# Optimization experiments

Hardware: AMD Instinct MI355X
Metric: run time of the kernel (lower is better)

Reference implementation:

```python
import jax, jax.numpy as jnp
import numpy as np

LOWRES = 256  # low-res input to coefficient tower
GB = 16       # spatial_bins (grid H=W)
LB = 8        # luma_bins (grid depth)
NIN, NOUT = 3, 3


def _conv_s2(x, w, b):
    # 3x3 stride-2 conv, torch padding=1
    y = jax.lax.conv_general_dilated(x, w, (2, 2), ((1, 1), (1, 1)),
                                     dimension_numbers=('NCHW', 'OIHW', 'NCHW'))
    return y + b[None, :, None, None]


def _pw(x, w, b):
    # 1x1 conv as einsum; w: [O, C]
    return jnp.einsum('bchw,oc->bohw', x, w) + b[None, :, None, None]


def _bilateral_slice(grid, guide, image):
    # grid [B,12,L,GH,GW]; guide [B,H,W] in [0,1]; image [B,NIN,H,W]
    B, C, L, GH, GW = grid.shape
    H, W = guide.shape[1], guide.shape[2]
    cx = (jnp.arange(W, dtype=jnp.float32) + 0.5) * (GW / W) - 0.5
    cy = (jnp.arange(H, dtype=jnp.float32) + 0.5) * (GH / H) - 0.5
    cz = guide * L - 0.5
    x0f = jnp.floor(cx); wx = cx - x0f
    y0f = jnp.floor(cy); wy = cy - y0f
    z0f = jnp.floor(cz); wz = cz - z0f
    x0 = x0f.astype(jnp.int32); y0 = y0f.astype(jnp.int32); z0 = z0f.astype(jnp.int32)
    bidx = jnp.arange(B)[:, None, None]
    acc = jnp.zeros((B, H, W, C), jnp.float32)
    for dz in (0, 1):
        zi = jnp.clip(z0 + dz, 0, L - 1)                     # [B,H,W]
        wzz = wz if dz else (1.0 - wz)
        for dy in (0, 1):
            yi = jnp.clip(y0 + dy, 0, GH - 1)[None, :, None]
            wyy = (wy if dy else (1.0 - wy))[None, :, None]
            for dx in (0, 1):
                xi = jnp.clip(x0 + dx, 0, GW - 1)[None, None, :]
                wxx = (wx if dx else (1.0 - wx))[None, None, :]
                g = grid[bidx, :, zi, yi, xi]                # [B,H,W,C]
                acc = acc + (wzz * wyy * wxx)[..., None] * g
    aff = acc.reshape(B, H, W, NOUT, NIN + 1)
    out = jnp.einsum('bhwci,bihw->bchw', aff[..., :NIN], image) \
        + jnp.transpose(aff[..., NIN], (0, 3, 1, 2))
    return out


def reference(image, val, sw0, sb0, sw1, sb1, sw2, sb2, sw3, sb3, spw, spb,
              lw1, lb1, lw2, lb2, lw3, lb3, cw, cb, fw1, fb1, fw2, fb2,
              gw, gb, ccm_w, ccm_b, shifts, slopes, prw, prb):
    B = image.shape[0]
    low = jax.image.resize(image, (B, NIN, LOWRES, LOWRES), 'bilinear', antialias=False)
    # splat tower: 4 stride-2 3x3 convs + final 1x1 (no relu)
    x = jax.nn.relu(_conv_s2(low, sw0, sb0))
    x = jax.nn.relu(_conv_s2(x, sw1, sb1))
    x = jax.nn.relu(_conv_s2(x, sw2, sb2))
    x = jax.nn.relu(_conv_s2(x, sw3, sb3))           # [B,64,16,16]
    splat = _pw(x, spw, spb) + val                   # + conditioning value
    # local path: three 1x1 convs with relu
    loc = jax.nn.relu(_pw(splat, lw1, lb1))
    loc = jax.nn.relu(_pw(loc, lw2, lb2))
    loc = jax.nn.relu(_pw(loc, lw3, lb3))            # [B,64,16,16]
    # condition path: 1x1 stride-2 conv -> adaptive avgpool(4) -> 2 fc layers
    c = jax.nn.relu(_pw(splat[:, :, ::2, ::2], cw, cb))  # [B,4,8,8]
    c = c.reshape(B, 4, 4, 2, 4, 2).mean(axis=(3, 5))    # [B,4,4,4]
    c = c.reshape(B, 64)
    c = jax.nn.relu(c @ fw1.T + fb1)
    c = jax.nn.relu(c @ fw2.T + fb2)                 # [B,64]
    fused = jax.nn.relu(c[:, :, None, None] + loc)
    coeff = _pw(fused, gw, gb)                       # [B,96,16,16]
    # split into LB chunks of 12 along channels, stack at dim 2
    grid = coeff.reshape(B, LB, NOUT * (NIN + 1), GB, GB).transpose(0, 2, 1, 3, 4)
    # guidemap: ccm -> piecewise-linear curve -> projection -> hardtanh [0,1]
    g = _pw(image, ccm_w, ccm_b)                     # [B,3,H,W]
    g = (slopes * jax.nn.relu(g[..., None] - shifts[None])).sum(-1)
    g = _pw(g, prw, prb)[:, 0]                       # [B,H,W]
    guide = jnp.clip(g, 0.0, 1.0)
    return _bilateral_slice(grid, guide, image)


def setup_inputs() -> dict:
    rng = np.random.default_rng(0)
    def rn(shape, fan_in):
        return jnp.asarray(rng.standard_normal(shape).astype(np.float32) * np.sqrt(2.0 / fan_in))
    B, H, W = 4, 1024, 1024
    d = {}
    d['image'] = jnp.asarray(rng.random((B, 3, H, W), dtype=np.float32))
    d['val'] = jnp.asarray(rng.random((B, 1, 1, 1), dtype=np.float32))
    # splat tower 3->8->16->32->64
    chans = [(3, 8), (8, 16), (16, 32), (32, 64)]
    for i, (ci, co) in enumerate(chans):
        d[f'sw{i}'] = rn((co, ci, 3, 3), ci * 9)
        d[f'sb{i}'] = jnp.zeros((co,), jnp.float32)
    d['spw'] = rn((64, 64), 64); d['spb'] = jnp.zeros((64,), jnp.float32)
    d['lw1'] = rn((128, 64), 64); d['lb1'] = jnp.zeros((128,), jnp.float32)
    d['lw2'] = rn((128, 128), 128); d['lb2'] = jnp.zeros((128,), jnp.float32)
    d['lw3'] = rn((64, 128), 128); d['lb3'] = jnp.zeros((64,), jnp.float32)
    d['cw'] = rn((4, 64), 64); d['cb'] = jnp.zeros((4,), jnp.float32)
    d['fw1'] = rn((64, 64), 64); d['fb1'] = jnp.zeros((64,), jnp.float32)
    d['fw2'] = rn((64, 64), 64); d['fb2'] = jnp.zeros((64,), jnp.float32)
    d['gw'] = rn((96, 64), 64); d['gb'] = jnp.zeros((96,), jnp.float32)
    # guide params (mirrors make_guide_params init)
    d['ccm_w'] = jnp.asarray(np.identity(3, dtype=np.float32)
                             + rng.standard_normal((3, 3)).astype(np.float32) * 1e-4)
    d['ccm_b'] = jnp.zeros((3,), jnp.float32)
    shifts = np.linspace(0, 1, 16, endpoint=False, dtype=np.float32)[None, None, None, :]
    d['shifts'] = jnp.asarray(np.tile(shifts, (3, 1, 1, 1)))
    slopes = np.zeros((1, 3, 1, 1, 16), dtype=np.float32); slopes[..., 0] = 1.0
    d['slopes'] = jnp.asarray(slopes)
    d['prw'] = jnp.ones((1, 3), jnp.float32) / 3.0
    d['prb'] = jnp.zeros((1,), jnp.float32)
    return d
```

## Files before the change

### kernel.cpp

```cpp
#include <hip/hip_runtime.h>

#define BATCH 4
#define HH 1024
#define WW 1024

__global__ __launch_bounds__(256) void dsconv0_k(const float* __restrict__ img,
                                                 const float* __restrict__ wgt,
                                                 const float* __restrict__ bias,
                                                 float* __restrict__ out) {
  int blk = blockIdx.x;
  int tx = blk & 7;
  int ty = (blk >> 3) & 7;
  int b = blk >> 6;
  int t = threadIdx.x;

  __shared__ float low[3][33][36];

  int Y0 = ty << 4, X0 = tx << 4;
  int gy0 = 2 * Y0 - 1, gx0 = 2 * X0 - 1;

  for (int i = t; i < 3 * 33 * 33; i += 256) {
    int c = i / 1089;
    int rem = i - c * 1089;
    int ly = rem / 33;
    int lx = rem - ly * 33;
    int gy = gy0 + ly, gx = gx0 + lx;
    float v = 0.f;
    if (gy >= 0 && gx >= 0) {
      const float* p = img + (size_t)(b * 3 + c) * HH * WW + (4 * gy + 1) * WW + 4 * gx + 1;
      v = 0.25f * (p[0] + p[1] + p[WW] + p[WW + 1]);
    }
    low[c][ly][lx] = v;
  }
  __syncthreads();

  int x = t & 15, y = t >> 4;
  float acc[8];
#pragma unroll
  for (int o = 0; o < 8; ++o) acc[o] = bias[o];
  for (int ci = 0; ci < 3; ++ci) {
#pragma unroll
    for (int ky = 0; ky < 3; ++ky) {
#pragma unroll
      for (int kx = 0; kx < 3; ++kx) {
        float v = low[ci][2 * y + ky][2 * x + kx];
#pragma unroll
        for (int o = 0; o < 8; ++o)
          acc[o] += wgt[o * 27 + ci * 9 + ky * 3 + kx] * v;
      }
    }
  }
  float* ob = out + (size_t)b * 8 * 128 * 128 + (Y0 + y) * 128 + X0 + x;
#pragma unroll
  for (int o = 0; o < 8; ++o) ob[o * 128 * 128] = fmaxf(acc[o], 0.f);
}

template <int CI, int CO, int HI, int P>
__global__ __launch_bounds__(256) void conv_tile_k(const float* __restrict__ in,
                                                   const float* __restrict__ wgt,
                                                   const float* __restrict__ bias,
                                                   float* __restrict__ out) {
  const int HO = HI / 2;
  const int NT = HO / P;
  const int HALO = 2 * P + 1;
  const int RS = 2 * P + 4;
  constexpr int NO = (CO * P * P) / 256;
  int blk = blockIdx.x;
  int tx = blk % NT;
  int ty = (blk / NT) % NT;
  int b = blk / (NT * NT);
  int t = threadIdx.x;

  __shared__ float s[CI][HALO][RS];

  int Y0 = ty * P, X0 = tx * P;
  int gy0 = 2 * Y0 - 1, gx0 = 2 * X0 - 1;

  for (int i = t; i < CI * HALO * HALO; i += 256) {
    int c = i / (HALO * HALO);
    int rem = i - c * (HALO * HALO);
    int ly = rem / HALO;
    int lx = rem - ly * HALO;
    int gy = gy0 + ly, gx = gx0 + lx;
    float v = 0.f;
    if (gy >= 0 && gy < HI && gx >= 0 && gx < HI)
      v = in[((size_t)(b * CI + c) * HI + gy) * HI + gx];
    s[c][ly][lx] = v;
  }
  __syncthreads();

  int px = t % (P * P);
  int og = t / (P * P);
  int x = px % P, y = px / P;
  float acc[NO];
#pragma unroll
  for (int j = 0; j < NO; ++j) acc[j] = bias[og * NO + j];
  for (int ci = 0; ci < CI; ++ci) {
#pragma unroll
    for (int ky = 0; ky < 3; ++ky) {
#pragma unroll
      for (int kx = 0; kx < 3; ++kx) {
        float v = s[ci][2 * y + ky][2 * x + kx];
#pragma unroll
        for (int j = 0; j < NO; ++j)
          acc[j] += wgt[((og * NO + j) * CI + ci) * 9 + ky * 3 + kx] * v;
      }
    }
  }
#pragma unroll
  for (int j = 0; j < NO; ++j)
    out[(size_t)(b * CO + og * NO + j) * HO * HO + (Y0 + y) * HO + X0 + x] =
        fmaxf(acc[j], 0.f);
}

__global__ __launch_bounds__(256) void cpfc_k(const float* __restrict__ x3,
                                              const float* __restrict__ spw,
                                              const float* __restrict__ spb,
                                              const float* __restrict__ val,
                                              const float* __restrict__ cw,
                                              const float* __restrict__ cb,
                                              const float* __restrict__ fw1,
                                              const float* __restrict__ fb1,
                                              const float* __restrict__ fw2,
                                              const float* __restrict__ fb2,
                                              float* __restrict__ fc2o) {
  __shared__ float eff[4][64];
  __shared__ float eb[4][4];
  __shared__ float sc[256];
  __shared__ float h1[256];
  int t = threadIdx.x;

  {
    int ch = t >> 6, k = t & 63;
    float a = 0.f;
#pragma unroll 8
    for (int c = 0; c < 64; ++c) a += cw[ch * 64 + c] * spw[c * 64 + k];
    eff[ch][k] = a;
  }
  if (t < 16) {
    int b = t >> 2, ch = t & 3;
    float a = cb[ch];
    float vb = val[b];
#pragma unroll 8
    for (int c = 0; c < 64; ++c) a += cw[ch * 64 + c] * (spb[c] + vb);
    eb[b][ch] = a;
  }
  __syncthreads();

  int b = t >> 6;
  int r = t & 63;
  int ch = r >> 4;
  int py = (r >> 2) & 3;
  int px = r & 3;
  float sum = 0.f;
  for (int dy = 0; dy < 2; ++dy)
    for (int dx = 0; dx < 2; ++dx) {
      int p = (py * 2 + dy) * 32 + (px * 2 + dx) * 2;
      float acc = eb[b][ch];
      const float* xb = x3 + ((size_t)b * 64) * 256 + p;
#pragma unroll 8
      for (int k = 0; k < 64; ++k) acc += eff[ch][k] * xb[k * 256];
      sum += fmaxf(acc, 0.f);
    }
  sc[t] = sum * 0.25f;
  __syncthreads();
  int o = t & 63;
  float acc = fb1[o];
#pragma unroll 8
  for (int k = 0; k < 64; ++k) acc += fw1[o * 64 + k] * sc[b * 64 + k];
  h1[t] = fmaxf(acc, 0.f);
  __syncthreads();
  acc = fb2[o];
#pragma unroll 8
  for (int k = 0; k < 64; ++k) acc += fw2[o * 64 + k] * h1[b * 64 + k];
  fc2o[t] = fmaxf(acc, 0.f);
}

template <int CI, int CO, int RELU>
__device__ __forceinline__ void pw_tile(const float (*__restrict__ X)[36],
                                        float (*__restrict__ Y)[36],
                                        const float* __restrict__ w,
                                        const float* __restrict__ bias,
                                        float badd, int t) {
  constexpr int NO = CO / 32;
  int pg = (t & 7) << 2;
  int og = t >> 3;
  float acc[NO][4];
#pragma unroll
  for (int j = 0; j < NO; ++j) {
    float bb = bias[og * NO + j] + badd;
#pragma unroll
    for (int u = 0; u < 4; ++u) acc[j][u] = bb;
  }
#pragma unroll 4
  for (int k = 0; k < CI; k += 4) {
    float4 xv0 = *(const float4*)&X[k][pg];
    float4 xv1 = *(const float4*)&X[k + 1][pg];
    float4 xv2 = *(const float4*)&X[k + 2][pg];
    float4 xv3 = *(const float4*)&X[k + 3][pg];
#pragma unroll
    for (int j = 0; j < NO; ++j) {
      float4 wv = *(const float4*)&w[(og * NO + j) * CI + k];
      acc[j][0] += wv.x * xv0.x + wv.y * xv1.x + wv.z * xv2.x + wv.w * xv3.x;
      acc[j][1] += wv.x * xv0.y + wv.y * xv1.y + wv.z * xv2.y + wv.w * xv3.y;
      acc[j][2] += wv.x * xv0.z + wv.y * xv1.z + wv.z * xv2.z + wv.w * xv3.z;
      acc[j][3] += wv.x * xv0.w + wv.y * xv1.w + wv.z * xv2.w + wv.w * xv3.w;
    }
  }
#pragma unroll
  for (int j = 0; j < NO; ++j) {
    int o = og * NO + j;
#pragma unroll
    for (int u = 0; u < 4; ++u) {
      float v = acc[j][u];
      if (RELU) v = fmaxf(v, 0.f);
      Y[o][pg + u] = v;
    }
  }
}

__global__ __launch_bounds__(256) void mlp_k(
    const float* __restrict__ x3, const float* __restrict__ spw,
    const float* __restrict__ spb, const float* __restrict__ val,
    const float* __restrict__ lw1, const float* __restrict__ lb1,
    const float* __restrict__ lw2, const float* __restrict__ lb2,
    const float* __restrict__ lw3, const float* __restrict__ lb3,
    const float* __restrict__ fc2o, const float* __restrict__ gw,
    const float* __restrict__ gb, float* __restrict__ gridt) {
  int blk = blockIdx.x;
  int b = blk >> 3;
  int p0 = (blk & 7) << 5;
  int t = threadIdx.x;

  __shared__ float A[128][36];
  __shared__ float Bf[128][36];

  for (int i = t; i < 64 * 32; i += 256) {
    int c = i >> 5, p = i & 31;
    A[c][p] = x3[((size_t)(b * 64 + c)) * 256 + p0 + p];
  }
  __syncthreads();

  pw_tile<64, 64, 0>(A, Bf, spw, spb, val[b], t);
  __syncthreads();
  pw_tile<64, 128, 1>(Bf, A, lw1, lb1, 0.f, t);
  __syncthreads();
  pw_tile<128, 128, 1>(A, Bf, lw2, lb2, 0.f, t);
  __syncthreads();
  pw_tile<128, 64, 1>(Bf, A, lw3, lb3, 0.f, t);
  __syncthreads();

  {
    int pg = (t & 7) << 2;
    int og = t >> 3;
    float acc[3][4];
#pragma unroll
    for (int j = 0; j < 3; ++j) {
      float bb = gb[og * 3 + j];
#pragma unroll
      for (int u = 0; u < 4; ++u) acc[j][u] = bb;
    }
    const float* cv = fc2o + b * 64;
#pragma unroll 4
    for (int k = 0; k < 64; k += 4) {
      float4 cc4 = *(const float4*)&cv[k];
      float4 xv0 = *(const float4*)&A[k][pg];
      float4 xv1 = *(const float4*)&A[k + 1][pg];
      float4 xv2 = *(const float4*)&A[k + 2][pg];
      float4 xv3 = *(const float4*)&A[k + 3][pg];
      xv0.x = fmaxf(xv0.x + cc4.x, 0.f); xv0.y = fmaxf(xv0.y + cc4.x, 0.f);
      xv0.z = fmaxf(xv0.z + cc4.x, 0.f); xv0.w = fmaxf(xv0.w + cc4.x, 0.f);
      xv1.x = fmaxf(xv1.x + cc4.y, 0.f); xv1.y = fmaxf(xv1.y + cc4.y, 0.f);
      xv1.z = fmaxf(xv1.z + cc4.y, 0.f); xv1.w = fmaxf(xv1.w + cc4.y, 0.f);
      xv2.x = fmaxf(xv2.x + cc4.z, 0.f); xv2.y = fmaxf(xv2.y + cc4.z, 0.f);
      xv2.z = fmaxf(xv2.z + cc4.z, 0.f); xv2.w = fmaxf(xv2.w + cc4.z, 0.f);
      xv3.x = fmaxf(xv3.x + cc4.w, 0.f); xv3.y = fmaxf(xv3.y + cc4.w, 0.f);
      xv3.z = fmaxf(xv3.z + cc4.w, 0.f); xv3.w = fmaxf(xv3.w + cc4.w, 0.f);
#pragma unroll
      for (int j = 0; j < 3; ++j) {
        float4 wv = *(const float4*)&gw[(og * 3 + j) * 64 + k];
        acc[j][0] += wv.x * xv0.x + wv.y * xv1.x + wv.z * xv2.x + wv.w * xv3.x;
        acc[j][1] += wv.x * xv0.y + wv.y * xv1.y + wv.z * xv2.y + wv.w * xv3.y;
        acc[j][2] += wv.x * xv0.z + wv.y * xv1.z + wv.z * xv2.z + wv.w * xv3.z;
        acc[j][3] += wv.x * xv0.w + wv.y * xv1.w + wv.z * xv2.w + wv.w * xv3.w;
      }
    }
#pragma unroll
    for (int j = 0; j < 3; ++j) {
      int o = og * 3 + j;
      int l = o / 12, cc = o - l * 12;
#pragma unroll
      for (int u = 0; u < 4; ++u)
        gridt[(size_t)(((b * 8 + l) << 8) + p0 + pg + u) * 12 + cc] = acc[j][u];
    }
  }
}

#define ZST 200
__global__ __launch_bounds__(256) void slice_k(
    const float* __restrict__ img, const float* __restrict__ gridt,
    const float* __restrict__ ccm_w, const float* __restrict__ ccm_b,
    const float* __restrict__ shifts, const float* __restrict__ slopes,
    const float* __restrict__ prw, const float* __restrict__ prb,
    float* __restrict__ out) {
  int blk = blockIdx.x;
  int b = blk >> 10;
  int h = blk & 1023;
  int t = threadIdx.x;

  __shared__ float sg[8 * ZST];
  __shared__ float2 lut[3][16];

  float cy = (h + 0.5f) * 0.015625f - 0.5f;
  float y0f = floorf(cy);
  float wy = cy - y0f;
  int y0 = (int)y0f;
  int yi0 = min(max(y0, 0), 15), yi1 = min(max(y0 + 1, 0), 15);

  if (t < 48) {
    int c = t >> 4, k = t & 15;
    float cs = 0.f, cbv = 0.f;
    for (int i = 0; i <= k; ++i) {
      float s = slopes[c * 16 + i];
      cs += s;
      cbv += s * shifts[c * 16 + i];
    }
    lut[c][k] = make_float2(cs, cbv);
  }

  for (int i = t; i < 384; i += 256) {
    int z = i / 48;
    int e = i - z * 48;
    const float4* s0 =
        (const float4*)(gridt + (size_t)(((b * 8 + z) << 8) + (yi0 << 4)) * 12);
    const float4* s1 =
        (const float4*)(gridt + (size_t)(((b * 8 + z) << 8) + (yi1 << 4)) * 12);
    float4 a = s0[e], c = s1[e];
    float4 v = make_float4(a.x + wy * (c.x - a.x), a.y + wy * (c.y - a.y),
                           a.z + wy * (c.z - a.z), a.w + wy * (c.w - a.w));
    *((float4*)(sg + z * ZST) + e) = v;
  }
  __syncthreads();

  int pp = (h << 10) + (t << 2);
  const float* ib = img + (size_t)b * 3 * HH * WW;
  float4 R4 = *(const float4*)(ib + pp);
  float4 G4 = *(const float4*)(ib + HH * WW + pp);
  float4 B4 = *(const float4*)(ib + 2 * HH * WW + pp);
  float r_[4] = {R4.x, R4.y, R4.z, R4.w};
  float g_[4] = {G4.x, G4.y, G4.z, G4.w};
  float b_[4] = {B4.x, B4.y, B4.z, B4.w};

  float m0 = ccm_w[0], m1 = ccm_w[1], m2 = ccm_w[2];
  float m3 = ccm_w[3], m4 = ccm_w[4], m5 = ccm_w[5];
  float m6 = ccm_w[6], m7 = ccm_w[7], m8 = ccm_w[8];
  float c0 = ccm_b[0], c1 = ccm_b[1], c2 = ccm_b[2];
  float p0 = prw[0], p1 = prw[1], p2 = prw[2], pb = prb[0];

  float base0 = shifts[0], base1 = shifts[16], base2 = shifts[32];
  float inv0 = 1.0f / (shifts[1] - base0);
  float inv1 = 1.0f / (shifts[17] - base1);
  float inv2 = 1.0f / (shifts[33] - base2);

  float ro[4], go[4], bo[4];
#pragma unroll
  for (int j = 0; j < 4; ++j) {
    float r = r_[j], g = g_[j], bl = b_[j];
    float v0 = c0 + m0 * r + m1 * g + m2 * bl;
    float v1 = c1 + m3 * r + m4 * g + m5 * bl;
    float v2 = c2 + m6 * r + m7 * g + m8 * bl;

    float tv0 = fmaxf(v0, base0);
    float tv1 = fmaxf(v1, base1);
    float tv2 = fmaxf(v2, base2);
    int j0 = min((int)((tv0 - base0) * inv0), 15);
    int j1 = min((int)((tv1 - base1) * inv1), 15);
    int j2 = min((int)((tv2 - base2) * inv2), 15);
    float2 e0 = lut[0][j0];
    float2 e1 = lut[1][j1];
    float2 e2 = lut[2][j2];
    float f0 = e0.x * tv0 - e0.y;
    float f1 = e1.x * tv1 - e1.y;
    float f2 = e2.x * tv2 - e2.y;

    float gg = pb + p0 * f0 + p1 * f1 + p2 * f2;
    float guide = fminf(fmaxf(gg, 0.f), 1.f);

    int w = (t << 2) + j;
    float cx = (w + 0.5f) * 0.015625f - 0.5f;
    float x0f = floorf(cx);
    float wx = cx - x0f;
    int x0i = (int)x0f;
    int xi0 = min(max(x0i, 0), 15), xi1 = min(max(x0i + 1, 0), 15);

    float cz = guide * 8.0f - 0.5f;
    float z0f = floorf(cz);
    float wz = cz - z0f;
    int z0i = (int)z0f;
    int zi0 = min(max(z0i, 0), 7), zi1 = min(max(z0i + 1, 0), 7);

    int oz0 = zi0 * ZST, oz1 = zi1 * ZST;
    int ox0 = xi0 * 12, ox1 = xi1 * 12;
    float wz1 = wz, wz0 = 1.f - wz;
    float wx1 = wx, wx0 = 1.f - wx;

    float acc[12];
#pragma unroll
    for (int k = 0; k < 12; ++k) acc[k] = 0.f;

#pragma unroll
    for (int dz = 0; dz < 2; ++dz) {
      int oz = dz ? oz1 : oz0;
      float wzz = dz ? wz1 : wz0;
#pragma unroll
      for (int dx = 0; dx < 2; ++dx) {
        int ox = dx ? ox1 : ox0;
        float wgt = wzz * (dx ? wx1 : wx0);
        const float* gp = sg + oz + ox;
        float4 a0 = *(const float4*)gp;
        float4 a1 = *(const float4*)(gp + 4);
        float4 a2 = *(const float4*)(gp + 8);
        acc[0] += wgt * a0.x;  acc[1] += wgt * a0.y;
        acc[2] += wgt * a0.z;  acc[3] += wgt * a0.w;
        acc[4] += wgt * a1.x;  acc[5] += wgt * a1.y;
        acc[6] += wgt * a1.z;  acc[7] += wgt * a1.w;
        acc[8] += wgt * a2.x;  acc[9] += wgt * a2.y;
        acc[10] += wgt * a2.z; acc[11] += wgt * a2.w;
      }
    }
    ro[j] = acc[0] * r + acc[1] * g + acc[2] * bl + acc[3];
    go[j] = acc[4] * r + acc[5] * g + acc[6] * bl + acc[7];
    bo[j] = acc[8] * r + acc[9] * g + acc[10] * bl + acc[11];
  }
  float* ob = out + (size_t)b * 3 * HH * WW;
  *(float4*)(ob + pp) = make_float4(ro[0], ro[1], ro[2], ro[3]);
  *(float4*)(ob + HH * WW + pp) = make_float4(go[0], go[1], go[2], go[3]);
  *(float4*)(ob + 2 * HH * WW + pp) = make_float4(bo[0], bo[1], bo[2], bo[3]);
}

extern "C" void kernel_launch(void* const* d_in, const int* in_sizes, int n_in,
                              void* d_out, int out_size, void* d_ws, size_t ws_size,
                              hipStream_t stream) {
  const float* image = (const float*)d_in[0];
  const float* val   = (const float*)d_in[1];
  const float* sw0 = (const float*)d_in[2];  const float* sb0 = (const float*)d_in[3];
  const float* sw1 = (const float*)d_in[4];  const float* sb1 = (const float*)d_in[5];
  const float* sw2 = (const float*)d_in[6];  const float* sb2 = (const float*)d_in[7];
  const float* sw3 = (const float*)d_in[8];  const float* sb3 = (const float*)d_in[9];
  const float* spw = (const float*)d_in[10]; const float* spb = (const float*)d_in[11];
  const float* lw1 = (const float*)d_in[12]; const float* lb1 = (const float*)d_in[13];
  const float* lw2 = (const float*)d_in[14]; const float* lb2 = (const float*)d_in[15];
  const float* lw3 = (const float*)d_in[16]; const float* lb3 = (const float*)d_in[17];
  const float* cw  = (const float*)d_in[18]; const float* cb  = (const float*)d_in[19];
  const float* fw1 = (const float*)d_in[20]; const float* fb1 = (const float*)d_in[21];
  const float* fw2 = (const float*)d_in[22]; const float* fb2 = (const float*)d_in[23];
  const float* gw  = (const float*)d_in[24]; const float* gb  = (const float*)d_in[25];
  const float* ccm_w = (const float*)d_in[26]; const float* ccm_b = (const float*)d_in[27];
  const float* shifts = (const float*)d_in[28]; const float* slopes = (const float*)d_in[29];
  const float* prw = (const float*)d_in[30]; const float* prb = (const float*)d_in[31];
  float* out = (float*)d_out;

  float* ws    = (float*)d_ws;
  float* x0    = ws;
  float* x1    = x0 + 524288;
  float* x2    = x1 + 262144;
  float* x3    = x2 + 131072;
  float* fc2o  = x3 + 65536;
  float* gridt = fc2o + 256;

  dsconv0_k<<<256, 256, 0, stream>>>(image, sw0, sb0, x0);
  conv_tile_k<8, 16, 128, 8><<<256, 256, 0, stream>>>(x0, sw1, sb1, x1);
  conv_tile_k<16, 32, 64, 4><<<256, 256, 0, stream>>>(x1, sw2, sb2, x2);
  conv_tile_k<32, 64, 32, 2><<<256, 256, 0, stream>>>(x2, sw3, sb3, x3);
  cpfc_k<<<1, 256, 0, stream>>>(x3, spw, spb, val, cw, cb, fw1, fb1, fw2, fb2,
                                fc2o);
  mlp_k<<<32, 256, 0, stream>>>(x3, spw, spb, val, lw1, lb1, lw2, lb2, lw3, lb3,
                                fc2o, gw, gb, gridt);
  slice_k<<<4096, 256, 0, stream>>>(image, gridt, ccm_w, ccm_b, shifts, slopes,
                                    prw, prb, out);
}
```

Measured before the change: 276.7 us.

## Parallelize global-feature conv/pool across blocks and fuse FC layers into MLP kernel

Replaces the single-block cpfc kernel with a 16-block cpool kernel, one block per (batch, channel), that splits the 64-wide reductions across four thread groups and then sums them. The two small fully-connected layers are moved into mlp_k, where each block recomputes them redundantly and overlaps them with the pointwise tile work. The aim is to shorten a serial, single-block stage on the critical path. The cost is duplicated FC work in all 32 mlp blocks and extra shared-memory reductions and syncs.

```diff
diff --git a/kernel.cpp b/kernel.cpp
--- a/kernel.cpp
+++ b/kernel.cpp
@@ -113,67 +113,62 @@
         fmaxf(acc[j], 0.f);
 }
 
-__global__ __launch_bounds__(256) void cpfc_k(const float* __restrict__ x3,
-                                              const float* __restrict__ spw,
-                                              const float* __restrict__ spb,
-                                              const float* __restrict__ val,
-                                              const float* __restrict__ cw,
-                                              const float* __restrict__ cb,
-                                              const float* __restrict__ fw1,
-                                              const float* __restrict__ fb1,
-                                              const float* __restrict__ fw2,
-                                              const float* __restrict__ fb2,
-                                              float* __restrict__ fc2o) {
-  __shared__ float eff[4][64];
-  __shared__ float eb[4][4];
-  __shared__ float sc[256];
-  __shared__ float h1[256];
+__global__ __launch_bounds__(256) void cpool_k(const float* __restrict__ x3,
+                                               const float* __restrict__ spw,
+                                               const float* __restrict__ spb,
+                                               const float* __restrict__ val,
+                                               const float* __restrict__ cw,
+                                               const float* __restrict__ cb,
+                                               float* __restrict__ cvec) {
+  int blk = blockIdx.x;
+  int ch = blk & 3, b = blk >> 2;
   int t = threadIdx.x;
+  int k = t & 63, q = t >> 6;
+
+  __shared__ float red[4][64];
+  __shared__ float red2[4];
+  __shared__ float effs[64];
+  __shared__ float s8[64];
+  __shared__ float ebs;
 
   {
-    int ch = t >> 6, k = t & 63;
     float a = 0.f;
-#pragma unroll 8
-    for (int c = 0; c < 64; ++c) a += cw[ch * 64 + c] * spw[c * 64 + k];
-    eff[ch][k] = a;
-  }
+#pragma unroll
+    for (int o = q * 16; o < q * 16 + 16; ++o)
+      a += cw[ch * 64 + o] * spw[o * 64 + k];
+    red[q][k] = a;
+  }
+  if (k == 0) {
+    float a = 0.f;
+    float vb = val[b];
+#pragma unroll
+    for (int o = q * 16; o < q * 16 + 16; ++o)
+      a += cw[ch * 64 + o] * (spb[o] + vb);
+    red2[q] = a;
+  }
+  __syncthreads();
+  if (t < 64) effs[t] = red[0][t] + red[1][t] + red[2][t] + red[3][t];
+  if (t == 0) ebs = cb[ch] + red2[0] + red2[1] + red2[2] + red2[3];
+  __syncthreads();
+
+  {
+    int p = ((k >> 3) << 5) + ((k & 7) << 1);
+    float a = 0.f;
+#pragma unroll
+    for (int kk = q * 16; kk < q * 16 + 16; ++kk)
+      a += effs[kk] * x3[((size_t)(b * 64 + kk)) * 256 + p];
+    red[q][k] = a;
+  }
+  __syncthreads();
+  if (t < 64)
+    s8[t] = fmaxf(red[0][t] + red[1][t] + red[2][t] + red[3][t] + ebs, 0.f);
+  __syncthreads();
   if (t < 16) {
-    int b = t >> 2, ch = t & 3;
-    float a = cb[ch];
-    float vb = val[b];
-#pragma unroll 8
-    for (int c = 0; c < 64; ++c) a += cw[ch * 64 + c] * (spb[c] + vb);
-    eb[b][ch] = a;
-  }
-  __syncthreads();
-
-  int b = t >> 6;
-  int r = t & 63;
-  int ch = r >> 4;
-  int py = (r >> 2) & 3;
-  int px = r & 3;
-  float sum = 0.f;
-  for (int dy = 0; dy < 2; ++dy)
-    for (int dx = 0; dx < 2; ++dx) {
-      int p = (py * 2 + dy) * 32 + (px * 2 + dx) * 2;
-      float acc = eb[b][ch];
-      const float* xb = x3 + ((size_t)b * 64) * 256 + p;
-#pragma unroll 8
-      for (int k = 0; k < 64; ++k) acc += eff[ch][k] * xb[k * 256];
-      sum += fmaxf(acc, 0.f);
-    }
-  sc[t] = sum * 0.25f;
-  __syncthreads();
-  int o = t & 63;
-  float acc = fb1[o];
-#pragma unroll 8
-  for (int k = 0; k < 64; ++k) acc += fw1[o * 64 + k] * sc[b * 64 + k];
-  h1[t] = fmaxf(acc, 0.f);
-  __syncthreads();
-  acc = fb2[o];
-#pragma unroll 8
-  for (int k = 0; k < 64; ++k) acc += fw2[o * 64 + k] * h1[b * 64 + k];
-  fc2o[t] = fmaxf(acc, 0.f);
+    int py = t >> 2, px = t & 3;
+    int i0 = (py * 2) * 8 + px * 2;
+    cvec[b * 64 + ch * 16 + t] =
+        0.25f * (s8[i0] + s8[i0 + 1] + s8[i0 + 8] + s8[i0 + 9]);
+  }
 }
 
 template <int CI, int CO, int RELU>
@@ -225,7 +220,9 @@
     const float* __restrict__ lw1, const float* __restrict__ lb1,
     const float* __restrict__ lw2, const float* __restrict__ lb2,
     const float* __restrict__ lw3, const float* __restrict__ lb3,
-    const float* __restrict__ fc2o, const float* __restrict__ gw,
+    const float* __restrict__ cvec, const float* __restrict__ fw1,
+    const float* __restrict__ fb1, const float* __restrict__ fw2,
+    const float* __restrict__ fb2, const float* __restrict__ gw,
     const float* __restrict__ gb, float* __restrict__ gridt) {
   int blk = blockIdx.x;
   int b = blk >> 3;
@@ -234,15 +231,29 @@
 
   __shared__ float A[128][36];
   __shared__ float Bf[128][36];
-
+  __shared__ float scv[64], h1v[64], f2v[64];
+
+  if (t < 64) scv[t] = cvec[b * 64 + t];
   for (int i = t; i < 64 * 32; i += 256) {
     int c = i >> 5, p = i & 31;
     A[c][p] = x3[((size_t)(b * 64 + c)) * 256 + p0 + p];
   }
   __syncthreads();
 
+  if (t < 64) {
+    float a = fb1[t];
+#pragma unroll 8
+    for (int k = 0; k < 64; ++k) a += fw1[t * 64 + k] * scv[k];
+    h1v[t] = fmaxf(a, 0.f);
+  }
   pw_tile<64, 64, 0>(A, Bf, spw, spb, val[b], t);
   __syncthreads();
+  if (t < 64) {
+    float a = fb2[t];
+#pragma unroll 8
+    for (int k = 0; k < 64; ++k) a += fw2[t * 64 + k] * h1v[k];
+    f2v[t] = fmaxf(a, 0.f);
+  }
   pw_tile<64, 128, 1>(Bf, A, lw1, lb1, 0.f, t);
   __syncthreads();
   pw_tile<128, 128, 1>(A, Bf, lw2, lb2, 0.f, t);
@@ -260,10 +271,9 @@
 #pragma unroll
       for (int u = 0; u < 4; ++u) acc[j][u] = bb;
     }
-    const float* cv = fc2o + b * 64;
 #pragma unroll 4
     for (int k = 0; k < 64; k += 4) {
-      float4 cc4 = *(const float4*)&cv[k];
+      float4 cc4 = *(const float4*)&f2v[k];
       float4 xv0 = *(const float4*)&A[k][pg];
       float4 xv1 = *(const float4*)&A[k + 1][pg];
       float4 xv2 = *(const float4*)&A[k + 2][pg];
@@ -465,17 +475,16 @@
   float* x1    = x0 + 524288;
   float* x2    = x1 + 262144;
   float* x3    = x2 + 131072;
-  float* fc2o  = x3 + 65536;
-  float* gridt = fc2o + 256;
+  float* cvec  = x3 + 65536;
+  float* gridt = cvec + 256;
 
   dsconv0_k<<<256, 256, 0, stream>>>(image, sw0, sb0, x0);
   conv_tile_k<8, 16, 128, 8><<<256, 256, 0, stream>>>(x0, sw1, sb1, x1);
   conv_tile_k<16, 32, 64, 4><<<256, 256, 0, stream>>>(x1, sw2, sb2, x2);
   conv_tile_k<32, 64, 32, 2><<<256, 256, 0, stream>>>(x2, sw3, sb3, x3);
-  cpfc_k<<<1, 256, 0, stream>>>(x3, spw, spb, val, cw, cb, fw1, fb1, fw2, fb2,
-                                fc2o);
+  cpool_k<<<16, 256, 0, stream>>>(x3, spw, spb, val, cw, cb, cvec);
   mlp_k<<<32, 256, 0, stream>>>(x3, spw, spb, val, lw1, lb1, lw2, lb2, lw3, lb3,
-                                fc2o, gw, gb, gridt);
+                                cvec, fw1, fb1, fw2, fb2, gw, gb, gridt);
   slice_k<<<4096, 256, 0, stream>>>(image, gridt, ccm_w, ccm_b, shifts, slopes,
                                     prw, prb, out);
 }
```

Measured after the change: 246.0 us. -11.1%, faster.
